# Kernel tuning notes

Measured on AMD Instinct MI355X. Metric: run time of the kernel, lower is better.

## Reference

```python
import jax, jax.numpy as jnp
import numpy as np

EPS = 1e-5  # config.layer_norm_epsilon


def setup_inputs() -> dict:
    key = jax.random.key(0)
    ks = jax.random.split(key, 7)
    B, S, D, K = 16, 2048, 768, 64
    return {
        "x": jax.random.normal(ks[0], (B, S, D), dtype=jnp.float32),
        "W_up": jax.random.normal(ks[1], (D, K), dtype=jnp.float32) * 0.02,
        "b_up": jax.random.normal(ks[2], (D,), dtype=jnp.float32) * 0.02,
        "W_down": jax.random.normal(ks[3], (K, D), dtype=jnp.float32) * 0.02,
        "b_down": jax.random.normal(ks[4], (K,), dtype=jnp.float32) * 0.02,
        "W_ln": 1.0 + 0.02 * jax.random.normal(ks[5], (D,), dtype=jnp.float32),
        "b_ln": 0.02 * jax.random.normal(ks[6], (D,), dtype=jnp.float32),
    }


def reference(x, W_up, b_up, W_down, b_down, W_ln, b_ln):
    # F.layer_norm with normalized_shape = x.size()[1:] -> normalize jointly
    # over (S, D) per batch element; W_ln/b_ln (shape [D]) broadcast to (S, D).
    mu = jnp.mean(x, axis=(1, 2), keepdims=True)            # [B,1,1]
    var = jnp.mean(jnp.square(x - mu), axis=(1, 2), keepdims=True)
    xn = (x - mu) * jax.lax.rsqrt(var + EPS) * W_ln + b_ln  # [B,S,D]
    # down-proj (no bias) -> ReLU -> up-proj (no bias) -> residual add
    h = jax.nn.relu(jnp.einsum('bsd,kd->bsk', xn, W_down))  # [B,S,K]
    return x + jnp.einsum('bsk,dk->bsd', h, W_up)           # [B,S,D]
```

## Files before the change

### kernel.cpp

```cpp
#include <hip/hip_runtime.h>

#define EPS   1e-5f
#define NB    16
#define NS    2048
#define ND    768
#define NK    64
#define NPB   (NS * ND)

typedef __attribute__((ext_vector_type(8))) short short8;
typedef __attribute__((ext_vector_type(4))) unsigned short ushort4v;
typedef __attribute__((ext_vector_type(4))) float f32x4;

#define LGKM_BAR() do {                                      \
    asm volatile("s_waitcnt lgkmcnt(0)" ::: "memory");       \
    __builtin_amdgcn_sched_barrier(0);                       \
    __builtin_amdgcn_s_barrier();                            \
} while (0)

static __device__ __forceinline__ short f2bf(float f) {
    unsigned u = __builtin_bit_cast(unsigned, f);
    u += 0x7fffu + ((u >> 16) & 1u);
    return (short)(u >> 16);
}
static __device__ __forceinline__ float bf2f(unsigned short h) {
    return __builtin_bit_cast(float, (unsigned)h << 16);
}

__global__ __launch_bounds__(256) void prep_reduce(
    const float* __restrict__ x, const float* __restrict__ W_up,
    const float* __restrict__ W_down, const float* __restrict__ W_ln,
    const float* __restrict__ b_ln, float2* __restrict__ stats_p,
    float* __restrict__ c1, float* __restrict__ c2,
    short* __restrict__ wdp, short* __restrict__ wub)
{
    __shared__ float red[8];
    const int bid = blockIdx.x, tid = threadIdx.x;
    const int wid = tid >> 6, lane = tid & 63;

    if (bid < 1024) {
        const int b = bid >> 6;
        const int chunk = bid & 63;
        const f32x4* xv = (const f32x4*)(x + (size_t)b * NPB + (size_t)chunk * (NPB / 64));
        float s = 0.f, ss = 0.f;
        #pragma unroll 8
        for (int i = tid; i < NPB / 64 / 4; i += 256) {
            f32x4 v = xv[i];
            s  += v[0] + v[1] + v[2] + v[3];
            ss += v[0]*v[0] + v[1]*v[1] + v[2]*v[2] + v[3]*v[3];
        }
        #pragma unroll
        for (int off = 32; off > 0; off >>= 1) {
            s  += __shfl_down(s, off, 64);
            ss += __shfl_down(ss, off, 64);
        }
        if (lane == 0) stats_p[bid * 4 + wid] = make_float2(s, ss);
    } else if (bid < 1088) {
        const int k = bid - 1024;
        float pc1 = 0.f, pc2 = 0.f;
        #pragma unroll
        for (int d = tid; d < ND; d += 256) {
            float wl = W_ln[d], wd = W_down[k * ND + d], bl = b_ln[d];
            wdp[k * ND + d] = f2bf(wl * wd);
            pc1 += wl * wd;
            pc2 += bl * wd;
        }
        #pragma unroll
        for (int off = 32; off > 0; off >>= 1) {
            pc1 += __shfl_down(pc1, off, 64);
            pc2 += __shfl_down(pc2, off, 64);
        }
        if (lane == 0) { red[wid] = pc1; red[4 + wid] = pc2; }
        __syncthreads();
        if (tid == 0) c1[k] = red[0] + red[1] + red[2] + red[3];
        if (tid == 1) c2[k] = red[4] + red[5] + red[6] + red[7];
    } else {
        const int i = (bid - 1088) * 256 + tid;
        wub[i] = f2bf(W_up[i]);
    }
}

__global__ __launch_bounds__(256) void fused_main(
    const float* __restrict__ x, const short* __restrict__ wdp,
    const short* __restrict__ wub, const float* __restrict__ c1,
    const float* __restrict__ c2, const float2* __restrict__ stats_p,
    float* __restrict__ out)
{
    __shared__ __align__(16) char lds[148480];

    const int tid  = threadIdx.x;
    const int wid  = tid >> 6;
    const int lane = tid & 63;
    const int r    = lane & 15;
    const int g    = lane >> 4;
    const int sw   = (r & 7) << 4;
    const int row0b = blockIdx.x * 64;
    const int row0  = row0b + wid * 16;
    const int b    = blockIdx.x >> 5;

    char* const XB  = lds;
    char* const WB  = lds + 98304;
    char* const HS  = lds + 131072;

    float s = 0.f, ss = 0.f;
    #pragma unroll
    for (int i = 0; i < 4; ++i) {
        float2 sp = stats_p[b * 256 + i * 64 + lane];
        s += sp.x; ss += sp.y;
    }
    #pragma unroll
    for (int off = 32; off > 0; off >>= 1) {
        s  += __shfl_xor(s, off, 64);
        ss += __shfl_xor(ss, off, 64);
    }
    const float invN = 1.f / (float)NPB;
    const float mu  = s * invN;
    const float var = ss * invN - mu * mu;
    const float rs  = rsqrtf(var + EPS);

    short8 bw[24];
    {
        const short* wr = wdp + (wid * 16 + r) * ND + g * 8;
        #pragma unroll
        for (int kk = 0; kk < 24; ++kk)
            bw[kk] = *(const short8*)(wr + kk * 32);
    }

    auto x_stage = [&](int c) {
        char* dst = XB + c * 24576;
        #pragma unroll
        for (int i = 0; i < 6; ++i) {
            int idx = i * 256 + tid;
            int row = idx / 24, u = idx % 24;
            const float* src = x + (size_t)(row0b + row) * ND + c * 192 + u * 8;
            f32x4 a0 = *(const f32x4*)(src);
            f32x4 a1 = *(const f32x4*)(src + 4);
            short8 h8;
            h8[0]=f2bf(a0[0]); h8[1]=f2bf(a0[1]); h8[2]=f2bf(a0[2]); h8[3]=f2bf(a0[3]);
            h8[4]=f2bf(a1[0]); h8[5]=f2bf(a1[1]); h8[6]=f2bf(a1[2]); h8[7]=f2bf(a1[3]);
            *(short8*)(dst + row * 384 + ((u * 16) ^ ((row & 7) << 4))) = h8;
        }
    };

    f32x4 acc[4] = {};
    auto g1_compute = [&](int c) {
        const char* X = XB + c * 24576;
        #pragma unroll
        for (int kk2 = 0; kk2 < 6; ++kk2) {
            const int kk = c * 6 + kk2;
            #pragma unroll
            for (int rt = 0; rt < 4; ++rt) {
                short8 af = *(const short8*)(X + (rt * 16 + r) * 384
                                               + ((kk2 * 64 + g * 16) ^ sw));
                acc[rt] = __builtin_amdgcn_mfma_f32_16x16x32_bf16(af, bw[kk], acc[rt], 0, 0, 0);
            }
        }
    };

    x_stage(0);
    LGKM_BAR();
    g1_compute(0);
    x_stage(1);
    LGKM_BAR();
    g1_compute(1);
    x_stage(2);
    LGKM_BAR();
    g1_compute(2);
    x_stage(3);
    LGKM_BAR();

    auto wub_load = [&](int w, short8* v) {
        #pragma unroll
        for (int i = 0; i < 4; ++i) {
            int idx = i * 256 + tid;
            int row = idx >> 3, u = idx & 7;
            v[i] = *(const short8*)(wub + (w * 128 + row) * 64 + u * 8);
        }
    };
    auto wub_write = [&](int p, const short8* v) {
        char* dst = WB + p * 16384;
        #pragma unroll
        for (int i = 0; i < 4; ++i) {
            int idx = i * 256 + tid;
            int row = idx >> 3, u = idx & 7;
            *(short8*)(dst + row * 128 + ((u * 16) ^ ((row & 7) << 4))) = v[i];
        }
    };

    {
        short8 u0[4];
        wub_load(0, u0);
        g1_compute(3);
        wub_write(0, u0);
    }

    {
        const int colg = wid * 16 + r;
        const float kb = c2[colg] - rs * mu * c1[colg];
        #pragma unroll
        for (int rt = 0; rt < 4; ++rt) {
            #pragma unroll
            for (int reg = 0; reg < 4; ++reg) {
                float z = fmaf(rs, acc[rt][reg], kb);
                const int hrow = rt * 16 + g * 4 + reg;
                *(short*)(HS + hrow * 128
                          + ((colg * 2) ^ ((hrow & 7) << 4))) = f2bf(fmaxf(z, 0.f));
            }
        }
    }
    LGKM_BAR();

    const char* H = HS + (wid * 16 + r) * 128;
    short8 a2_0 = *(const short8*)(H + ((g * 16) ^ sw));
    short8 a2_1 = *(const short8*)(H + ((64 + g * 16) ^ sw));
    LGKM_BAR();

    float*    outr = out + (size_t)row0 * ND;
    const int erow = lane >> 4;
    const int ecol = (lane & 15) * 4;
    float* S = (float*)(HS) + wid * 1088;

    for (int w = 0; w < 6; ++w) {
        short8 u[4];
        if (w < 5) wub_load(w + 1, u);
        const char* W = WB + (w & 1) * 16384;
        #pragma unroll
        for (int dq = 0; dq < 2; ++dq) {
            const int dcg = w * 2 + dq;
            f32x4 acc2[4] = {};
            #pragma unroll
            for (int cf = 0; cf < 4; ++cf) {
                const int dl = dq * 64 + cf * 16 + r;
                short8 b0 = *(const short8*)(W + dl * 128 + ((g * 16) ^ sw));
                short8 b1 = *(const short8*)(W + dl * 128 + ((64 + g * 16) ^ sw));
                acc2[cf] = __builtin_amdgcn_mfma_f32_16x16x32_bf16(a2_0, b0, acc2[cf], 0, 0, 0);
                acc2[cf] = __builtin_amdgcn_mfma_f32_16x16x32_bf16(a2_1, b1, acc2[cf], 0, 0, 0);
            }
            #pragma unroll
            for (int cf = 0; cf < 4; ++cf)
                #pragma unroll
                for (int reg = 0; reg < 4; ++reg)
                    S[(g * 4 + reg) * 68 + cf * 16 + r] = acc2[cf][reg];
            #pragma unroll
            for (int j = 0; j < 4; ++j) {
                const int row   = j * 4 + erow;
                f32x4 v = *(const f32x4*)(S + row * 68 + ecol);
                const int col   = dcg * 64 + ecol;
                const int row_l = wid * 16 + row;
                const int c     = col / 192;
                const int wb    = (col - c * 192) * 2;
                const char* xa  = XB + c * 24576 + row_l * 384
                                  + (((wb & ~15) ^ ((row_l & 7) << 4)) | (wb & 15));
                ushort4v hx = *(const ushort4v*)xa;
                v[0] += bf2f(hx[0]); v[1] += bf2f(hx[1]);
                v[2] += bf2f(hx[2]); v[3] += bf2f(hx[3]);
                __builtin_nontemporal_store(v, (f32x4*)(outr + (size_t)row * ND + col));
            }
        }
        if (w < 5) wub_write((w + 1) & 1, u);
        LGKM_BAR();
    }
}

extern "C" void kernel_launch(void* const* d_in, const int* in_sizes, int n_in,
                              void* d_out, int out_size, void* d_ws, size_t ws_size,
                              hipStream_t stream)
{
    const float* x      = (const float*)d_in[0];
    const float* W_up   = (const float*)d_in[1];
    const float* W_down = (const float*)d_in[3];
    const float* W_ln   = (const float*)d_in[5];
    const float* b_ln   = (const float*)d_in[6];
    float* out = (float*)d_out;

    char* ws = (char*)d_ws;
    float2* stats_p = (float2*)ws;
    float*  c1      = (float*)(ws + 32768);
    float*  c2      = (float*)(ws + 33024);
    short*  wdp     = (short*)(ws + 33280);
    short*  wub     = (short*)(ws + 131584);

    prep_reduce<<<1280, 256, 0, stream>>>(x, W_up, W_down, W_ln, b_ln,
                                          stats_p, c1, c2, wdp, wub);
    fused_main<<<512, 256, 0, stream>>>(x, wdp, wub, c1, c2, stats_p, out);
}
```

Before: 57.92 us.

## Process two row tiles per block and prefetch next tile's x during output phase

Halves the grid so each block handles two consecutive 64-row tiles. While the first tile's up-projection and residual store runs, the block stages the second tile's x chunks into LDS slots it has already finished reading. This overlaps global loads with the store phase and replaces two waves of one-block-per-CU work with a single persistent-like wave. It also amortizes the per-block stats reduction and W_down register load over two tiles. The cost is a longer serial chain per block, more complex LDS reuse ordering, and lower parallelism if fewer blocks fit than CUs.

```diff
diff --git a/kernel.cpp b/kernel.cpp
--- a/kernel.cpp
+++ b/kernel.cpp
@@ -79,7 +79,7 @@
     }
 }
 
-__global__ __launch_bounds__(256) void fused_main(
+__global__ __launch_bounds__(256) void fused_pair(
     const float* __restrict__ x, const short* __restrict__ wdp,
     const short* __restrict__ wub, const float* __restrict__ c1,
     const float* __restrict__ c2, const float2* __restrict__ stats_p,
@@ -93,45 +93,21 @@
     const int r    = lane & 15;
     const int g    = lane >> 4;
     const int sw   = (r & 7) << 4;
-    const int row0b = blockIdx.x * 64;
-    const int row0  = row0b + wid * 16;
-    const int b    = blockIdx.x >> 5;
+    const int rb0  = blockIdx.x * 128;
+    const int rb1  = rb0 + 64;
+    const int b    = blockIdx.x >> 4;
 
     char* const XB  = lds;
     char* const WB  = lds + 98304;
     char* const HS  = lds + 131072;
 
-    float s = 0.f, ss = 0.f;
-    #pragma unroll
-    for (int i = 0; i < 4; ++i) {
-        float2 sp = stats_p[b * 256 + i * 64 + lane];
-        s += sp.x; ss += sp.y;
-    }
-    #pragma unroll
-    for (int off = 32; off > 0; off >>= 1) {
-        s  += __shfl_xor(s, off, 64);
-        ss += __shfl_xor(ss, off, 64);
-    }
-    const float invN = 1.f / (float)NPB;
-    const float mu  = s * invN;
-    const float var = ss * invN - mu * mu;
-    const float rs  = rsqrtf(var + EPS);
-
-    short8 bw[24];
-    {
-        const short* wr = wdp + (wid * 16 + r) * ND + g * 8;
-        #pragma unroll
-        for (int kk = 0; kk < 24; ++kk)
-            bw[kk] = *(const short8*)(wr + kk * 32);
-    }
-
-    auto x_stage = [&](int c) {
+    auto x_stage = [&](int c, int rb) {
         char* dst = XB + c * 24576;
         #pragma unroll
         for (int i = 0; i < 6; ++i) {
             int idx = i * 256 + tid;
             int row = idx / 24, u = idx % 24;
-            const float* src = x + (size_t)(row0b + row) * ND + c * 192 + u * 8;
+            const float* src = x + (size_t)(rb + row) * ND + c * 192 + u * 8;
             f32x4 a0 = *(const f32x4*)(src);
             f32x4 a1 = *(const f32x4*)(src + 4);
             short8 h8;
@@ -141,7 +117,38 @@
         }
     };
 
-    f32x4 acc[4] = {};
+    x_stage(0, rb0);
+
+    float s = 0.f, ss = 0.f;
+    #pragma unroll
+    for (int i = 0; i < 4; ++i) {
+        float2 sp = stats_p[b * 256 + i * 64 + lane];
+        s += sp.x; ss += sp.y;
+    }
+    #pragma unroll
+    for (int off = 32; off > 0; off >>= 1) {
+        s  += __shfl_xor(s, off, 64);
+        ss += __shfl_xor(ss, off, 64);
+    }
+    const float invN = 1.f / (float)NPB;
+    const float mu  = s * invN;
+    const float var = ss * invN - mu * mu;
+    const float rs  = rsqrtf(var + EPS);
+
+    short8 bw[24];
+    {
+        const short* wr = wdp + (wid * 16 + r) * ND + g * 8;
+        #pragma unroll
+        for (int kk = 0; kk < 24; ++kk)
+            bw[kk] = *(const short8*)(wr + kk * 32);
+    }
+
+    f32x4 acc[4];
+    #pragma unroll
+    for (int rt = 0; rt < 4; ++rt)
+        #pragma unroll
+        for (int q = 0; q < 4; ++q) acc[rt][q] = 0.f;
+
     auto g1_compute = [&](int c) {
         const char* X = XB + c * 24576;
         #pragma unroll
@@ -156,18 +163,6 @@
         }
     };
 
-    x_stage(0);
-    LGKM_BAR();
-    g1_compute(0);
-    x_stage(1);
-    LGKM_BAR();
-    g1_compute(1);
-    x_stage(2);
-    LGKM_BAR();
-    g1_compute(2);
-    x_stage(3);
-    LGKM_BAR();
-
     auto wub_load = [&](int w, short8* v) {
         #pragma unroll
         for (int i = 0; i < 4; ++i) {
@@ -186,79 +181,120 @@
         }
     };
 
+    const int erow = lane >> 4;
+    const int ecol = (lane & 15) * 4;
+
+    auto do_tail = [&](int rb, int rb_next) {
+        {
+            const int colg = wid * 16 + r;
+            const float kb = c2[colg] - rs * mu * c1[colg];
+            #pragma unroll
+            for (int rt = 0; rt < 4; ++rt) {
+                #pragma unroll
+                for (int reg = 0; reg < 4; ++reg) {
+                    float z = fmaf(rs, acc[rt][reg], kb);
+                    const int hrow = rt * 16 + g * 4 + reg;
+                    *(short*)(HS + hrow * 128
+                              + ((colg * 2) ^ ((hrow & 7) << 4))) = f2bf(fmaxf(z, 0.f));
+                }
+            }
+        }
+        LGKM_BAR();
+
+        const char* H = HS + (wid * 16 + r) * 128;
+        short8 a2_0 = *(const short8*)(H + ((g * 16) ^ sw));
+        short8 a2_1 = *(const short8*)(H + ((64 + g * 16) ^ sw));
+        LGKM_BAR();
+
+        float* outr = out + (size_t)(rb + wid * 16) * ND;
+        float* S = (float*)(HS) + wid * 1088;
+
+        for (int w = 0; w < 6; ++w) {
+            if (rb_next >= 0) {
+                if      (w == 2) x_stage(0, rb_next);
+                else if (w == 3) x_stage(1, rb_next);
+                else if (w == 5) x_stage(2, rb_next);
+            }
+            short8 u[4];
+            if (w < 5) wub_load(w + 1, u);
+            const char* W = WB + (w & 1) * 16384;
+            #pragma unroll
+            for (int dq = 0; dq < 2; ++dq) {
+                const int dcg = w * 2 + dq;
+                f32x4 acc2[4];
+                #pragma unroll
+                for (int cf = 0; cf < 4; ++cf)
+                    #pragma unroll
+                    for (int q = 0; q < 4; ++q) acc2[cf][q] = 0.f;
+                #pragma unroll
+                for (int cf = 0; cf < 4; ++cf) {
+                    const int dl = dq * 64 + cf * 16 + r;
+                    short8 b0 = *(const short8*)(W + dl * 128 + ((g * 16) ^ sw));
+                    short8 b1 = *(const short8*)(W + dl * 128 + ((64 + g * 16) ^ sw));
+                    acc2[cf] = __builtin_amdgcn_mfma_f32_16x16x32_bf16(a2_0, b0, acc2[cf], 0, 0, 0);
+                    acc2[cf] = __builtin_amdgcn_mfma_f32_16x16x32_bf16(a2_1, b1, acc2[cf], 0, 0, 0);
+                }
+                #pragma unroll
+                for (int cf = 0; cf < 4; ++cf)
+                    #pragma unroll
+                    for (int reg = 0; reg < 4; ++reg)
+                        S[(g * 4 + reg) * 68 + cf * 16 + r] = acc2[cf][reg];
+                #pragma unroll
+                for (int j = 0; j < 4; ++j) {
+                    const int row   = j * 4 + erow;
+                    f32x4 v = *(const f32x4*)(S + row * 68 + ecol);
+                    const int col   = dcg * 64 + ecol;
+                    const int row_l = wid * 16 + row;
+                    const int c     = col / 192;
+                    const int wb    = (col - c * 192) * 2;
+                    const char* xa  = XB + c * 24576 + row_l * 384
+                                      + (((wb & ~15) ^ ((row_l & 7) << 4)) | (wb & 15));
+                    ushort4v hx = *(const ushort4v*)xa;
+                    v[0] += bf2f(hx[0]); v[1] += bf2f(hx[1]);
+                    v[2] += bf2f(hx[2]); v[3] += bf2f(hx[3]);
+                    __builtin_nontemporal_store(v, (f32x4*)(outr + (size_t)row * ND + col));
+                }
+            }
+            if (w < 5) wub_write((w + 1) & 1, u);
+            LGKM_BAR();
+        }
+    };
+
+    LGKM_BAR();
+    g1_compute(0);
+    x_stage(1, rb0);
+    LGKM_BAR();
+    g1_compute(1);
+    x_stage(2, rb0);
+    LGKM_BAR();
+    g1_compute(2);
+    x_stage(3, rb0);
+    LGKM_BAR();
     {
         short8 u0[4];
         wub_load(0, u0);
         g1_compute(3);
         wub_write(0, u0);
     }
-
+    do_tail(rb0, rb1);
+
+    #pragma unroll
+    for (int rt = 0; rt < 4; ++rt)
+        #pragma unroll
+        for (int q = 0; q < 4; ++q) acc[rt][q] = 0.f;
+
+    x_stage(3, rb1);
+    g1_compute(0);
+    g1_compute(1);
+    g1_compute(2);
+    LGKM_BAR();
     {
-        const int colg = wid * 16 + r;
-        const float kb = c2[colg] - rs * mu * c1[colg];
-        #pragma unroll
-        for (int rt = 0; rt < 4; ++rt) {
-            #pragma unroll
-            for (int reg = 0; reg < 4; ++reg) {
-                float z = fmaf(rs, acc[rt][reg], kb);
-                const int hrow = rt * 16 + g * 4 + reg;
-                *(short*)(HS + hrow * 128
-                          + ((colg * 2) ^ ((hrow & 7) << 4))) = f2bf(fmaxf(z, 0.f));
-            }
-        }
-    }
-    LGKM_BAR();
-
-    const char* H = HS + (wid * 16 + r) * 128;
-    short8 a2_0 = *(const short8*)(H + ((g * 16) ^ sw));
-    short8 a2_1 = *(const short8*)(H + ((64 + g * 16) ^ sw));
-    LGKM_BAR();
-
-    float*    outr = out + (size_t)row0 * ND;
-    const int erow = lane >> 4;
-    const int ecol = (lane & 15) * 4;
-    float* S = (float*)(HS) + wid * 1088;
-
-    for (int w = 0; w < 6; ++w) {
-        short8 u[4];
-        if (w < 5) wub_load(w + 1, u);
-        const char* W = WB + (w & 1) * 16384;
-        #pragma unroll
-        for (int dq = 0; dq < 2; ++dq) {
-            const int dcg = w * 2 + dq;
-            f32x4 acc2[4] = {};
-            #pragma unroll
-            for (int cf = 0; cf < 4; ++cf) {
-                const int dl = dq * 64 + cf * 16 + r;
-                short8 b0 = *(const short8*)(W + dl * 128 + ((g * 16) ^ sw));
-                short8 b1 = *(const short8*)(W + dl * 128 + ((64 + g * 16) ^ sw));
-                acc2[cf] = __builtin_amdgcn_mfma_f32_16x16x32_bf16(a2_0, b0, acc2[cf], 0, 0, 0);
-                acc2[cf] = __builtin_amdgcn_mfma_f32_16x16x32_bf16(a2_1, b1, acc2[cf], 0, 0, 0);
-            }
-            #pragma unroll
-            for (int cf = 0; cf < 4; ++cf)
-                #pragma unroll
-                for (int reg = 0; reg < 4; ++reg)
-                    S[(g * 4 + reg) * 68 + cf * 16 + r] = acc2[cf][reg];
-            #pragma unroll
-            for (int j = 0; j < 4; ++j) {
-                const int row   = j * 4 + erow;
-                f32x4 v = *(const f32x4*)(S + row * 68 + ecol);
-                const int col   = dcg * 64 + ecol;
-                const int row_l = wid * 16 + row;
-                const int c     = col / 192;
-                const int wb    = (col - c * 192) * 2;
-                const char* xa  = XB + c * 24576 + row_l * 384
-                                  + (((wb & ~15) ^ ((row_l & 7) << 4)) | (wb & 15));
-                ushort4v hx = *(const ushort4v*)xa;
-                v[0] += bf2f(hx[0]); v[1] += bf2f(hx[1]);
-                v[2] += bf2f(hx[2]); v[3] += bf2f(hx[3]);
-                __builtin_nontemporal_store(v, (f32x4*)(outr + (size_t)row * ND + col));
-            }
-        }
-        if (w < 5) wub_write((w + 1) & 1, u);
-        LGKM_BAR();
-    }
+        short8 u0[4];
+        wub_load(0, u0);
+        g1_compute(3);
+        wub_write(0, u0);
+    }
+    do_tail(rb1, -1);
 }
 
 extern "C" void kernel_launch(void* const* d_in, const int* in_sizes, int n_in,
@@ -281,5 +317,5 @@
 
     prep_reduce<<<1280, 256, 0, stream>>>(x, W_up, W_down, W_ln, b_ln,
                                           stats_p, c1, c2, wdp, wub);
-    fused_main<<<512, 256, 0, stream>>>(x, wdp, wub, c1, c2, stats_p, out);
-}
+    fused_pair<<<256, 256, 0, stream>>>(x, wdp, wub, c1, c2, stats_p, out);
+}
```

Result: slower. 63.76 us (+10.1%).
